# Kernel optimization log

Measured on AMD Instinct MI355X. Metric: run time of the kernel, lower is better.

Reference implementation:

```python
import jax, jax.numpy as jnp
import numpy as np

N_NODES = 50000
N_EDGES = 800000
HIDDEN = 64
NUM_FEATURES = 1
OUT_DIM = 2


def setup_inputs() -> dict:
    key = jax.random.key(0)
    k = jax.random.split(key, 6)
    x = jax.random.normal(k[0], (N_NODES, NUM_FEATURES), dtype=jnp.float32)
    edge_index = jax.random.randint(k[1], (2, N_EDGES), 0, N_NODES, dtype=jnp.int32)
    # GCNConv params (PyG default: glorot weight, zero bias; random here for testing)
    W1 = jax.random.normal(k[2], (NUM_FEATURES, HIDDEN), dtype=jnp.float32) * 0.5
    b1 = jax.random.normal(k[3], (HIDDEN,), dtype=jnp.float32) * 0.1
    W2 = jax.random.normal(k[4], (HIDDEN, OUT_DIM), dtype=jnp.float32) * 0.1
    b2 = jax.random.normal(k[5], (OUT_DIM,), dtype=jnp.float32) * 0.1
    return {"x": x, "edge_index": edge_index, "W1": W1, "b1": b1, "W2": W2, "b2": b2}


def _gcn_norm(edge_index, num_nodes):
    # PyG gcn_norm with add_self_loops=True, symmetric normalization
    row, col = edge_index[0], edge_index[1]
    loop = jnp.arange(num_nodes, dtype=row.dtype)
    row = jnp.concatenate([row, loop])
    col = jnp.concatenate([col, loop])
    ew = jnp.ones(row.shape[0], dtype=jnp.float32)
    deg = jax.ops.segment_sum(ew, col, num_segments=num_nodes)  # in-degree incl. self-loop
    dinv = jnp.where(deg > 0, jax.lax.rsqrt(deg), 0.0)
    norm = dinv[row] * dinv[col]  # [E+N]
    return row, col, norm


def _gcn_conv(x, row, col, norm, W, b, num_nodes):
    h = x @ W                                  # [N, out] transform first (out <= in here is fine)
    msg = h[row] * norm[:, None]               # gather + scale, [E+N, out]
    out = jax.ops.segment_sum(msg, col, num_segments=num_nodes)  # scatter-add at targets
    return out + b


def reference(x, edge_index, W1, b1, W2, b2):
    row, col, norm = _gcn_norm(edge_index, N_NODES)
    h = _gcn_conv(x, row, col, norm, W1, b1, N_NODES)
    h = jax.nn.relu(h)
    out = _gcn_conv(h, row, col, norm, W2, b2, N_NODES)
    return out
```

## Files before the change

### kernel.cpp

```cpp
#include <hip/hip_runtime.h>
#include <math.h>

#define N_NODES 50000
#define N_EDGES 800000
#define HIDDEN  64
#define NBUCK   32
#define SLICE   1568
#define BCAP    26500
#define NBB     64
#define EPB     (N_EDGES / NBB)
#define TILE    2048
#define NSUB    8
#define NGROUP  (N_NODES / 4)


__global__ __launch_bounds__(256)
void k_bucket(const int* __restrict__ row, const int* __restrict__ col,
              unsigned* __restrict__ tails, unsigned* __restrict__ histPart,
              unsigned* __restrict__ bks) {
    __shared__ unsigned hist[NGROUP];
    __shared__ unsigned stage[TILE];
    __shared__ unsigned char sbuck[TILE];
    __shared__ unsigned cntb[NBUCK], baseb[NBUCK], cnt2[NBUCK], gpos[NBUCK];
    const int t  = threadIdx.x;
    const int e0 = blockIdx.x * EPB;

    for (int i = t; i < NGROUP; i += 256) hist[i] = 0u;

    for (int tile = 0; tile < EPB; tile += TILE) {
        const int cnt = min(TILE, EPB - tile);
        if (t < NBUCK) { cntb[t] = 0u; cnt2[t] = 0u; }
        __syncthreads();

        int myc[8], myr[8], mb[8];
#pragma unroll
        for (int k = 0; k < 8; ++k) {
            int ii = k * 256 + t;
            mb[k] = -1;
            if (ii < cnt) {
                int c = col[e0 + tile + ii];
                int r = row[e0 + tile + ii];
                myc[k] = c; myr[k] = r;
                int b = c / SLICE;
                mb[k] = b;
                atomicAdd(&cntb[b], 1u);
                atomicAdd(&hist[c >> 2], 1u << ((c & 3) * 8));
            }
        }
        __syncthreads();
        if (t == 0) {
            unsigned acc = 0;
            for (int b = 0; b < NBUCK; ++b) { baseb[b] = acc; acc += cntb[b]; }
        }
        __syncthreads();
#pragma unroll
        for (int k = 0; k < 8; ++k) {
            if (mb[k] >= 0) {
                unsigned off = atomicAdd(&cnt2[mb[k]], 1u);
                unsigned pos = baseb[mb[k]] + off;
                stage[pos] = ((unsigned)(myc[k] % SLICE) << 16) | (unsigned)myr[k];
                sbuck[pos] = (unsigned char)mb[k];
            }
        }
        __syncthreads();
        if (t < NBUCK) gpos[t] = atomicAdd(&tails[t], cntb[t]);
        __syncthreads();
        for (int i = t; i < cnt; i += 256) {
            int b = sbuck[i];
            unsigned dst = gpos[b] + ((unsigned)i - baseb[b]);
            if (dst < BCAP) bks[(size_t)b * BCAP + dst] = stage[i];
        }
        __syncthreads();
    }
    unsigned* hp = histPart + (size_t)blockIdx.x * NGROUP;
    for (int i = t; i < NGROUP; i += 256) hp[i] = hist[i];
}

__global__ __launch_bounds__(256)
void k_g(const unsigned* __restrict__ histPart, const float* __restrict__ x,
         float* __restrict__ dinv, float* __restrict__ g) {
    int i = blockIdx.x * 256 + threadIdx.x;
    if (i >= NGROUP) return;
    unsigned sum = 0;
    for (int b0 = 0; b0 < NBB; b0 += 8) {
        unsigned v[8];
#pragma unroll
        for (int k = 0; k < 8; ++k) v[k] = histPart[(size_t)(b0 + k) * NGROUP + i];
#pragma unroll
        for (int k = 0; k < 8; ++k) sum += v[k];
    }
    int n0 = i * 4;
#pragma unroll
    for (int b = 0; b < 4; ++b) {
        int deg = (int)((sum >> (8 * b)) & 255u);
        float di = rsqrtf((float)(deg + 1));
        dinv[n0 + b] = di;
        g[n0 + b] = di * x[n0 + b];
    }
}

__global__ __launch_bounds__(256)
void k_agg1(const unsigned* __restrict__ bks, const unsigned* __restrict__ tails,
            const float* __restrict__ g, float* __restrict__ part1) {
    __shared__ float acc[SLICE];
    const int b = blockIdx.x >> 3;
    const int s = blockIdx.x & (NSUB - 1);
    for (int i = threadIdx.x; i < SLICE; i += 256) acc[i] = 0.0f;
    __syncthreads();
    unsigned tail = min(tails[b], (unsigned)BCAP);
    unsigned chunk = (tail + NSUB - 1) / NSUB;
    unsigned lo = s * chunk, hi = min(lo + chunk, tail);
    const unsigned* bk = bks + (size_t)b * BCAP;
    for (unsigned i = lo + threadIdx.x; i < hi; i += 256) {
        unsigned v = bk[i];
        atomicAdd(&acc[v >> 16], g[v & 0xFFFFu]);
    }
    __syncthreads();
    float* dst = part1 + ((size_t)b * NSUB + s) * SLICE;
    for (int i = threadIdx.x; i < SLICE; i += 256) dst[i] = acc[i];
}

__global__ __launch_bounds__(256)
void k_mlp(const float* __restrict__ part1, const float* __restrict__ g,
           const float* __restrict__ dinv,
           const float* __restrict__ W1, const float* __restrict__ b1,
           const float* __restrict__ W2, float2* __restrict__ z) {
    int n = blockIdx.x * 256 + threadIdx.x;
    if (n >= N_NODES) return;
    int b = n / SLICE, cl = n % SLICE;
    const float* p = part1 + (size_t)b * NSUB * SLICE + cl;
    float t = 0.0f;
#pragma unroll
    for (int s = 0; s < NSUB; ++s) t += p[(size_t)s * SLICE];
    float di = dinv[n];
    float sv = di * (t + g[n]);
    float y0 = 0.0f, y1 = 0.0f;
#pragma unroll
    for (int k = 0; k < HIDDEN; ++k) {
        float h = fmaxf(sv * W1[k] + b1[k], 0.0f);
        y0 += h * W2[2 * k];
        y1 += h * W2[2 * k + 1];
    }
    z[n] = make_float2(di * y0, di * y1);
}

__global__ __launch_bounds__(256)
void k_agg2(const unsigned* __restrict__ bks, const unsigned* __restrict__ tails,
            const float2* __restrict__ z, float2* __restrict__ part2) {
    __shared__ float accx[SLICE];
    __shared__ float accy[SLICE];
    const int b = blockIdx.x >> 3;
    const int s = blockIdx.x & (NSUB - 1);
    for (int i = threadIdx.x; i < SLICE; i += 256) { accx[i] = 0.0f; accy[i] = 0.0f; }
    __syncthreads();
    unsigned tail = min(tails[b], (unsigned)BCAP);
    unsigned chunk = (tail + NSUB - 1) / NSUB;
    unsigned lo = s * chunk, hi = min(lo + chunk, tail);
    const unsigned* bk = bks + (size_t)b * BCAP;
    for (unsigned i = lo + threadIdx.x; i < hi; i += 256) {
        unsigned v = bk[i];
        float2 zz = z[v & 0xFFFFu];
        atomicAdd(&accx[v >> 16], zz.x);
        atomicAdd(&accy[v >> 16], zz.y);
    }
    __syncthreads();
    float2* dst = part2 + ((size_t)b * NSUB + s) * SLICE;
    for (int i = threadIdx.x; i < SLICE; i += 256) dst[i] = make_float2(accx[i], accy[i]);
}

__global__ __launch_bounds__(256)
void k_final(const float2* __restrict__ part2, const float2* __restrict__ z,
             const float* __restrict__ dinv, const float* __restrict__ b2,
             float2* __restrict__ out) {
    int n = blockIdx.x * 256 + threadIdx.x;
    if (n >= N_NODES) return;
    int b = n / SLICE, cl = n % SLICE;
    const float2* p = part2 + (size_t)b * NSUB * SLICE + cl;
    float Tx = 0.0f, Ty = 0.0f;
#pragma unroll
    for (int s = 0; s < NSUB; ++s) { float2 v = p[(size_t)s * SLICE]; Tx += v.x; Ty += v.y; }
    float di = dinv[n];
    float2 zn = z[n];
    out[n] = make_float2(di * (Tx + zn.x) + b2[0], di * (Ty + zn.y) + b2[1]);
}


extern "C" void kernel_launch(void* const* d_in, const int* in_sizes, int n_in,
                              void* d_out, int out_size, void* d_ws, size_t ws_size,
                              hipStream_t stream) {
    const float* x  = (const float*)d_in[0];
    const int*   ei = (const int*)d_in[1];
    const float* W1 = (const float*)d_in[2];
    const float* b1 = (const float*)d_in[3];
    const float* W2 = (const float*)d_in[4];
    const float* b2 = (const float*)d_in[5];

    const int* row = ei;
    const int* col = ei + N_EDGES;

    char* p = (char*)d_ws;
    unsigned* tails    = (unsigned*)p;                     p += 64 * 4;
    unsigned* histPart = (unsigned*)p;                     p += (size_t)NBB * NGROUP * 4;
    unsigned* bks      = (unsigned*)p;                     p += (size_t)NBUCK * BCAP * 4;
    float*    part1    = (float*)p;                        p += (size_t)NBUCK * NSUB * SLICE * 4;
    float2*   part2    = (float2*)p;                       p += (size_t)NBUCK * NSUB * SLICE * 8;
    float*    dinv     = (float*)p;                        p += N_NODES * 4;
    float*    g        = (float*)p;                        p += N_NODES * 4;
    float2*   z        = (float2*)p;

    const int gG = (NGROUP + 255) / 256;
    const int gN = (N_NODES + 255) / 256;
    const int gA = NBUCK * NSUB;

    hipMemsetAsync(tails, 0, 64 * sizeof(unsigned), stream);
    k_bucket<<<NBB, 256, 0, stream>>>(row, col, tails, histPart, bks);
    k_g     <<<gG,  256, 0, stream>>>(histPart, x, dinv, g);
    k_agg1  <<<gA,  256, 0, stream>>>(bks, tails, g, part1);
    k_mlp   <<<gN,  256, 0, stream>>>(part1, g, dinv, W1, b1, W2, z);
    k_agg2  <<<gA,  256, 0, stream>>>(bks, tails, z, part2);
    k_final <<<gN,  256, 0, stream>>>(part2, z, dinv, b2, (float2*)d_out);
}
```

Before: 133.3 us.

## Split edge bucketing across 256 single-pass blocks instead of 64 tiled blocks

The bucketing and degree-histogram kernel now runs 256 blocks, each partitioning a 3125-edge chunk in one pass, instead of 64 blocks looping over 2048-edge tiles. This aims to fill far more compute units during the partition stage and to drop the per-tile synchronisation loop. In exchange, the per-block degree histograms grow fourfold, so the histogram-reduction kernel writes and reads much more global memory. Column indices are also read twice, and the bucket capacity is trimmed slightly. The remaining edits rename variables and simplify index arithmetic.

```diff
diff --git a/kernel.cpp b/kernel.cpp
--- a/kernel.cpp
+++ b/kernel.cpp
@@ -4,88 +4,73 @@
 #define N_NODES 50000
 #define N_EDGES 800000
 #define HIDDEN  64
+#define NGROUP  12500
+#define NPART   256
+#define PCHUNK  (N_EDGES / NPART)
 #define NBUCK   32
 #define SLICE   1568
-#define BCAP    26500
-#define NBB     64
-#define EPB     (N_EDGES / NBB)
-#define TILE    2048
+#define BCAP    26000
 #define NSUB    8
-#define NGROUP  (N_NODES / 4)
-
-
-__global__ __launch_bounds__(256)
-void k_bucket(const int* __restrict__ row, const int* __restrict__ col,
-              unsigned* __restrict__ tails, unsigned* __restrict__ histPart,
-              unsigned* __restrict__ bks) {
+
+
+__global__ __launch_bounds__(256)
+void k_part(const int* __restrict__ row, const int* __restrict__ col,
+            unsigned* __restrict__ tails, unsigned* __restrict__ histPart,
+            unsigned* __restrict__ bks) {
     __shared__ unsigned hist[NGROUP];
-    __shared__ unsigned stage[TILE];
-    __shared__ unsigned char sbuck[TILE];
+    __shared__ unsigned stage[PCHUNK];
+    __shared__ unsigned char sb[PCHUNK];
     __shared__ unsigned cntb[NBUCK], baseb[NBUCK], cnt2[NBUCK], gpos[NBUCK];
     const int t  = threadIdx.x;
-    const int e0 = blockIdx.x * EPB;
+    const int e0 = blockIdx.x * PCHUNK;
 
     for (int i = t; i < NGROUP; i += 256) hist[i] = 0u;
-
-    for (int tile = 0; tile < EPB; tile += TILE) {
-        const int cnt = min(TILE, EPB - tile);
-        if (t < NBUCK) { cntb[t] = 0u; cnt2[t] = 0u; }
-        __syncthreads();
-
-        int myc[8], myr[8], mb[8];
-#pragma unroll
-        for (int k = 0; k < 8; ++k) {
-            int ii = k * 256 + t;
-            mb[k] = -1;
-            if (ii < cnt) {
-                int c = col[e0 + tile + ii];
-                int r = row[e0 + tile + ii];
-                myc[k] = c; myr[k] = r;
-                int b = c / SLICE;
-                mb[k] = b;
-                atomicAdd(&cntb[b], 1u);
-                atomicAdd(&hist[c >> 2], 1u << ((c & 3) * 8));
-            }
-        }
-        __syncthreads();
-        if (t == 0) {
-            unsigned acc = 0;
-            for (int b = 0; b < NBUCK; ++b) { baseb[b] = acc; acc += cntb[b]; }
-        }
-        __syncthreads();
-#pragma unroll
-        for (int k = 0; k < 8; ++k) {
-            if (mb[k] >= 0) {
-                unsigned off = atomicAdd(&cnt2[mb[k]], 1u);
-                unsigned pos = baseb[mb[k]] + off;
-                stage[pos] = ((unsigned)(myc[k] % SLICE) << 16) | (unsigned)myr[k];
-                sbuck[pos] = (unsigned char)mb[k];
-            }
-        }
-        __syncthreads();
-        if (t < NBUCK) gpos[t] = atomicAdd(&tails[t], cntb[t]);
-        __syncthreads();
-        for (int i = t; i < cnt; i += 256) {
-            int b = sbuck[i];
-            unsigned dst = gpos[b] + ((unsigned)i - baseb[b]);
-            if (dst < BCAP) bks[(size_t)b * BCAP + dst] = stage[i];
-        }
-        __syncthreads();
-    }
+    if (t < NBUCK) { cntb[t] = 0u; cnt2[t] = 0u; }
+    __syncthreads();
+
+    for (int i = t; i < PCHUNK; i += 256) {
+        int c = col[e0 + i];
+        atomicAdd(&hist[c >> 2], 1u << ((c & 3) * 8));
+        atomicAdd(&cntb[c / SLICE], 1u);
+    }
+    __syncthreads();
+    if (t == 0) {
+        unsigned acc = 0;
+        for (int b = 0; b < NBUCK; ++b) { baseb[b] = acc; acc += cntb[b]; }
+    }
+    __syncthreads();
+    for (int i = t; i < PCHUNK; i += 256) {
+        int c = col[e0 + i];
+        int r = row[e0 + i];
+        int b = c / SLICE;
+        unsigned off = atomicAdd(&cnt2[b], 1u);
+        unsigned pos = baseb[b] + off;
+        stage[pos] = ((unsigned)(c - b * SLICE) << 16) | (unsigned)r;
+        sb[pos] = (unsigned char)b;
+    }
+    __syncthreads();
+    if (t < NBUCK) gpos[t] = atomicAdd(&tails[t], cntb[t]);
+    __syncthreads();
+    for (int i = t; i < PCHUNK; i += 256) {
+        int b = sb[i];
+        unsigned dst = gpos[b] + ((unsigned)i - baseb[b]);
+        if (dst < BCAP) bks[(size_t)b * BCAP + dst] = stage[i];
+    }
+    __syncthreads();
     unsigned* hp = histPart + (size_t)blockIdx.x * NGROUP;
     for (int i = t; i < NGROUP; i += 256) hp[i] = hist[i];
 }
 
 __global__ __launch_bounds__(256)
-void k_g(const unsigned* __restrict__ histPart, const float* __restrict__ x,
+void k_g(const unsigned* __restrict__ part, const float* __restrict__ x,
          float* __restrict__ dinv, float* __restrict__ g) {
     int i = blockIdx.x * 256 + threadIdx.x;
     if (i >= NGROUP) return;
     unsigned sum = 0;
-    for (int b0 = 0; b0 < NBB; b0 += 8) {
+    for (int c0 = 0; c0 < NPART; c0 += 8) {
         unsigned v[8];
 #pragma unroll
-        for (int k = 0; k < 8; ++k) v[k] = histPart[(size_t)(b0 + k) * NGROUP + i];
+        for (int k = 0; k < 8; ++k) v[k] = part[(size_t)(c0 + k) * NGROUP + i];
 #pragma unroll
         for (int k = 0; k < 8; ++k) sum += v[k];
     }
@@ -116,7 +101,7 @@
         atomicAdd(&acc[v >> 16], g[v & 0xFFFFu]);
     }
     __syncthreads();
-    float* dst = part1 + ((size_t)b * NSUB + s) * SLICE;
+    float* dst = part1 + (size_t)blockIdx.x * SLICE;
     for (int i = threadIdx.x; i < SLICE; i += 256) dst[i] = acc[i];
 }
 
@@ -127,7 +112,7 @@
            const float* __restrict__ W2, float2* __restrict__ z) {
     int n = blockIdx.x * 256 + threadIdx.x;
     if (n >= N_NODES) return;
-    int b = n / SLICE, cl = n % SLICE;
+    int b = n / SLICE, cl = n - b * SLICE;
     const float* p = part1 + (size_t)b * NSUB * SLICE + cl;
     float t = 0.0f;
 #pragma unroll
@@ -147,11 +132,11 @@
 __global__ __launch_bounds__(256)
 void k_agg2(const unsigned* __restrict__ bks, const unsigned* __restrict__ tails,
             const float2* __restrict__ z, float2* __restrict__ part2) {
-    __shared__ float accx[SLICE];
-    __shared__ float accy[SLICE];
+    __shared__ float ax[SLICE];
+    __shared__ float ay[SLICE];
     const int b = blockIdx.x >> 3;
     const int s = blockIdx.x & (NSUB - 1);
-    for (int i = threadIdx.x; i < SLICE; i += 256) { accx[i] = 0.0f; accy[i] = 0.0f; }
+    for (int i = threadIdx.x; i < SLICE; i += 256) { ax[i] = 0.0f; ay[i] = 0.0f; }
     __syncthreads();
     unsigned tail = min(tails[b], (unsigned)BCAP);
     unsigned chunk = (tail + NSUB - 1) / NSUB;
@@ -160,12 +145,13 @@
     for (unsigned i = lo + threadIdx.x; i < hi; i += 256) {
         unsigned v = bk[i];
         float2 zz = z[v & 0xFFFFu];
-        atomicAdd(&accx[v >> 16], zz.x);
-        atomicAdd(&accy[v >> 16], zz.y);
-    }
-    __syncthreads();
-    float2* dst = part2 + ((size_t)b * NSUB + s) * SLICE;
-    for (int i = threadIdx.x; i < SLICE; i += 256) dst[i] = make_float2(accx[i], accy[i]);
+        unsigned cl = v >> 16;
+        atomicAdd(&ax[cl], zz.x);
+        atomicAdd(&ay[cl], zz.y);
+    }
+    __syncthreads();
+    float2* dst = part2 + (size_t)blockIdx.x * SLICE;
+    for (int i = threadIdx.x; i < SLICE; i += 256) dst[i] = make_float2(ax[i], ay[i]);
 }
 
 __global__ __launch_bounds__(256)
@@ -174,11 +160,14 @@
              float2* __restrict__ out) {
     int n = blockIdx.x * 256 + threadIdx.x;
     if (n >= N_NODES) return;
-    int b = n / SLICE, cl = n % SLICE;
+    int b = n / SLICE, cl = n - b * SLICE;
     const float2* p = part2 + (size_t)b * NSUB * SLICE + cl;
     float Tx = 0.0f, Ty = 0.0f;
 #pragma unroll
-    for (int s = 0; s < NSUB; ++s) { float2 v = p[(size_t)s * SLICE]; Tx += v.x; Ty += v.y; }
+    for (int s = 0; s < NSUB; ++s) {
+        float2 v = p[(size_t)s * SLICE];
+        Tx += v.x; Ty += v.y;
+    }
     float di = dinv[n];
     float2 zn = z[n];
     out[n] = make_float2(di * (Tx + zn.x) + b2[0], di * (Ty + zn.y) + b2[1]);
@@ -199,24 +188,24 @@
     const int* col = ei + N_EDGES;
 
     char* p = (char*)d_ws;
-    unsigned* tails    = (unsigned*)p;                     p += 64 * 4;
-    unsigned* histPart = (unsigned*)p;                     p += (size_t)NBB * NGROUP * 4;
-    unsigned* bks      = (unsigned*)p;                     p += (size_t)NBUCK * BCAP * 4;
-    float*    part1    = (float*)p;                        p += (size_t)NBUCK * NSUB * SLICE * 4;
-    float2*   part2    = (float2*)p;                       p += (size_t)NBUCK * NSUB * SLICE * 8;
-    float*    dinv     = (float*)p;                        p += N_NODES * 4;
-    float*    g        = (float*)p;                        p += N_NODES * 4;
+    unsigned* tails    = (unsigned*)p;  p += 128;
+    unsigned* histPart = (unsigned*)p;  p += (size_t)NPART * NGROUP * 4;
+    unsigned* bks      = (unsigned*)p;  p += (size_t)NBUCK * BCAP * 4;
+    float*    part1    = (float*)p;     p += (size_t)NBUCK * NSUB * SLICE * 4;
+    float2*   part2    = (float2*)p;    p += (size_t)NBUCK * NSUB * SLICE * 8;
+    float*    dinv     = (float*)p;     p += N_NODES * 4;
+    float*    g        = (float*)p;     p += N_NODES * 4;
     float2*   z        = (float2*)p;
 
     const int gG = (NGROUP + 255) / 256;
     const int gN = (N_NODES + 255) / 256;
     const int gA = NBUCK * NSUB;
 
-    hipMemsetAsync(tails, 0, 64 * sizeof(unsigned), stream);
-    k_bucket<<<NBB, 256, 0, stream>>>(row, col, tails, histPart, bks);
-    k_g     <<<gG,  256, 0, stream>>>(histPart, x, dinv, g);
-    k_agg1  <<<gA,  256, 0, stream>>>(bks, tails, g, part1);
-    k_mlp   <<<gN,  256, 0, stream>>>(part1, g, dinv, W1, b1, W2, z);
-    k_agg2  <<<gA,  256, 0, stream>>>(bks, tails, z, part2);
-    k_final <<<gN,  256, 0, stream>>>(part2, z, dinv, b2, (float2*)d_out);
-}
+    hipMemsetAsync(tails, 0, NBUCK * sizeof(unsigned), stream);
+    k_part <<<NPART, 256, 0, stream>>>(row, col, tails, histPart, bks);
+    k_g    <<<gG,    256, 0, stream>>>(histPart, x, dinv, g);
+    k_agg1 <<<gA,    256, 0, stream>>>(bks, tails, g, part1);
+    k_mlp  <<<gN,    256, 0, stream>>>(part1, g, dinv, W1, b1, W2, z);
+    k_agg2 <<<gA,    256, 0, stream>>>(bks, tails, z, part2);
+    k_final<<<gN,    256, 0, stream>>>(part2, z, dinv, b2, (float2*)d_out);
+}
```

New measurement: 126.1 us. 1.06x faster.
